# Kernel tuning notes

Hardware: AMD Instinct MI355X
Metric: run time of the kernel (lower is better)

Reference implementation:

```python
import jax, jax.numpy as jnp
import numpy as np

N = 50          # n_nodes
TAU = 1.0       # sinkhorn_tau
ITERS = 5       # sinkhorn_iters
ALPHA = 1.0


def _psi_fn(x, W1, b1, W2, b2):
    # x: [B, N, F]
    h = jax.nn.leaky_relu(x @ W1 + b1)          # [B, N, H], slope 0.01 matches torch default
    M = jax.nn.leaky_relu(h @ W2 + b2)          # [B, N, N]
    P = jnp.exp(M / TAU)
    for _ in range(ITERS):                      # alternating row/col normalization
        P = P / jnp.sum(P, axis=2, keepdims=True)
        P = P / jnp.sum(P, axis=1, keepdims=True)
    return P


def _hungarian(cost):
    """O(n^3) Hungarian (shortest augmenting path, like scipy.linear_sum_assignment).
    cost: [n, n] numpy. Returns col index assigned to each row (minimizes cost)."""
    n = cost.shape[0]
    INF = 1e18
    u = np.zeros(n + 1)
    v = np.zeros(n + 1)
    p = np.zeros(n + 1, dtype=np.int64)   # p[j] = row matched to column j (1-based)
    for i in range(1, n + 1):
        p[0] = i
        j0 = 0
        minv = np.full(n + 1, INF)
        way = np.zeros(n + 1, dtype=np.int64)
        used = np.zeros(n + 1, dtype=bool)
        while True:
            used[j0] = True
            i0 = p[j0]
            cur = cost[i0 - 1, :] - u[i0] - v[1:]
            free = ~used[1:]
            better = free & (cur < minv[1:])
            mv = minv[1:]
            mv[better] = cur[better]
            way[1:][better] = j0
            cand = np.where(free, mv, INF)
            j1 = int(np.argmin(cand)) + 1
            delta = cand[j1 - 1]
            u[p[used]] += delta
            v[used] -= delta
            mv[free] -= delta
            j0 = j1
            if p[j0] == 0:
                break
        while j0 != 0:
            j1 = way[j0]
            p[j0] = p[j1]
            j0 = j1
    row_to_col = np.zeros(n, dtype=np.int64)
    for j in range(1, n + 1):
        if p[j] > 0:
            row_to_col[p[j] - 1] = j - 1
    return row_to_col


def setup_inputs() -> dict:
    key = jax.random.key(0)
    k1, k2, k3, k4, k5 = jax.random.split(key, 5)
    B, F, H = 128, 1024, 4096
    s1 = 1.0 / np.sqrt(F)
    s2 = 1.0 / np.sqrt(H)
    x = jax.random.normal(k1, (B, N, F), dtype=jnp.float32)
    W1 = jax.random.uniform(k2, (F, H), minval=-s1, maxval=s1, dtype=jnp.float32)
    b1 = jax.random.uniform(k3, (H,), minval=-s1, maxval=s1, dtype=jnp.float32)
    W2 = jax.random.uniform(k4, (H, N), minval=-s2, maxval=s2, dtype=jnp.float32)
    b2 = jax.random.uniform(k5, (N,), minval=-s2, maxval=s2, dtype=jnp.float32)
    return {"x": x, "W1": W1, "b1": b1, "W2": W2, "b2": b2, "do_round": 1}


def reference(x, W1, b1, W2, b2, do_round):
    psi = _psi_fn(x, W1, b1, W2, b2)            # [B, N, N] doubly-stochastic (approx)
    if do_round:
        batch = np.asarray(psi)
        B = batch.shape[0]
        perms_np = np.zeros((B, N, N), dtype=np.float32)
        rows = np.arange(N)
        for i in range(B):
            cols = _hungarian(-batch[i])        # maximize psi == minimize -psi
            perms_np[i, rows, cols] = 1.0
        perms = jnp.asarray(perms_np)
        dist = jnp.sum(psi * perms, axis=(1, 2)) / N   # [B]
        X = (1.0 - ALPHA) * perms + ALPHA * psi
        return (psi, perms, X, dist)
    return (psi, None, None, None)
```

## Files before the change

### kernel.cpp

```cpp
#include <hip/hip_runtime.h>

#define NMAT 50
#define BATCH 128
#define FDIM 1024
#define HDIM 4096
#define ROWS 6400
#define PSIZE 320000
#define NPART 8
#define HINF 1e18

#define WS_M_OFF   0
#define WS_XH_OFF  20480000LL
#define WS_XL_OFF  33587200LL
#define WS_W1H_OFF 46694400LL
#define WS_W1L_OFF 55083008LL
#define WS_W2P_OFF 63471616LL
#define WS_H_OFF   64520192LL
#define WS_MIN     (WS_H_OFF + 128LL * HDIM * 4)

typedef __bf16 bf16x8 __attribute__((ext_vector_type(8)));
typedef float f32x4 __attribute__((ext_vector_type(4)));
typedef double f64x4 __attribute__((ext_vector_type(4)));
typedef unsigned short u16;

__device__ __forceinline__ float bf16_to_f32(unsigned short h) {
  return __uint_as_float(((unsigned int)h) << 16);
}
__device__ __forceinline__ unsigned short f32_to_bf16(float f) {
  unsigned int u = __float_as_uint(f);
  u += 0x7FFFu + ((u >> 16) & 1u);
  return (unsigned short)(u >> 16);
}

__device__ __forceinline__ void gload16(const u16* g, u16* l) {
  __builtin_amdgcn_global_load_lds(
      (const __attribute__((address_space(1))) unsigned int*)g,
      (__attribute__((address_space(3))) unsigned int*)l, 16, 0, 0);
}

__device__ __forceinline__ double wave_min_f64(double x) {
  union { double d; int i[2]; } u, t;
  u.d = x;
#define DPP_MIN_STEP(ctrl)                                                   \
  t.i[0] = __builtin_amdgcn_update_dpp(u.i[0], u.i[0], ctrl, 0xf, 0xf, false);\
  t.i[1] = __builtin_amdgcn_update_dpp(u.i[1], u.i[1], ctrl, 0xf, 0xf, false);\
  u.d = fmin(u.d, t.d);
  DPP_MIN_STEP(0x111)
  DPP_MIN_STEP(0x112)
  DPP_MIN_STEP(0x114)
  DPP_MIN_STEP(0x118)
  DPP_MIN_STEP(0x142)
  DPP_MIN_STEP(0x143)
#undef DPP_MIN_STEP
  union { double d; int i[2]; } r;
  r.i[0] = __builtin_amdgcn_readlane(u.i[0], 63);
  r.i[1] = __builtin_amdgcn_readlane(u.i[1], 63);
  return r.d;
}

__global__ __launch_bounds__(256) void convert_x(
    const float* __restrict__ X, u16* __restrict__ Xh, u16* __restrict__ Xl) {
  int t = threadIdx.x;
  int mt = blockIdx.x >> 5, k0b = blockIdx.x & 31;
  size_t outbase = (size_t)blockIdx.x * 4096;
#pragma unroll
  for (int it = 0; it < 2; ++it) {
    int idx = t + it * 256;
    int m = idx & 127, kg = idx >> 7;
    const float* src = X + (size_t)(mt * 128 + m) * FDIM + k0b * 32 + kg * 8;
    float4 v0 = *(const float4*)src;
    float4 v1 = *(const float4*)(src + 4);
    float f[8] = {v0.x, v0.y, v0.z, v0.w, v1.x, v1.y, v1.z, v1.w};
    unsigned short h[8], l[8];
#pragma unroll
    for (int j = 0; j < 8; ++j) {
      h[j] = f32_to_bf16(f[j]);
      l[j] = f32_to_bf16(f[j] - bf16_to_f32(h[j]));
    }
    uint4 hv, lv;
    hv.x = h[0] | ((unsigned)h[1] << 16); hv.y = h[2] | ((unsigned)h[3] << 16);
    hv.z = h[4] | ((unsigned)h[5] << 16); hv.w = h[6] | ((unsigned)h[7] << 16);
    lv.x = l[0] | ((unsigned)l[1] << 16); lv.y = l[2] | ((unsigned)l[3] << 16);
    lv.z = l[4] | ((unsigned)l[5] << 16); lv.w = l[6] | ((unsigned)l[7] << 16);
    size_t off = outbase + (size_t)(kg * 128 + m) * 8;
    *(uint4*)&Xh[off] = hv;
    *(uint4*)&Xl[off] = lv;
  }
}

__global__ __launch_bounds__(256) void convert_w1(
    const float* __restrict__ W1, u16* __restrict__ Wh, u16* __restrict__ Wl) {
  int t = threadIdx.x;
  int nt = blockIdx.x >> 5, k0b = blockIdx.x & 31;
  size_t outbase = (size_t)blockIdx.x * 4096;
#pragma unroll
  for (int it = 0; it < 2; ++it) {
    int idx = t + it * 256;
    int n = idx & 127, kg = idx >> 7;
    float f[8];
#pragma unroll
    for (int j = 0; j < 8; ++j)
      f[j] = W1[(size_t)(k0b * 32 + kg * 8 + j) * HDIM + nt * 128 + n];
    unsigned short h[8], l[8];
#pragma unroll
    for (int j = 0; j < 8; ++j) {
      h[j] = f32_to_bf16(f[j]);
      l[j] = f32_to_bf16(f[j] - bf16_to_f32(h[j]));
    }
    uint4 hv, lv;
    hv.x = h[0] | ((unsigned)h[1] << 16); hv.y = h[2] | ((unsigned)h[3] << 16);
    hv.z = h[4] | ((unsigned)h[5] << 16); hv.w = h[6] | ((unsigned)h[7] << 16);
    lv.x = l[0] | ((unsigned)l[1] << 16); lv.y = l[2] | ((unsigned)l[3] << 16);
    lv.z = l[4] | ((unsigned)l[5] << 16); lv.w = l[6] | ((unsigned)l[7] << 16);
    size_t off = outbase + (size_t)(kg * 128 + n) * 8;
    *(uint4*)&Wh[off] = hv;
    *(uint4*)&Wl[off] = lv;
  }
}

__global__ __launch_bounds__(256) void convert_w2(
    const float* __restrict__ W2, float* __restrict__ W2p) {
  int idx = blockIdx.x * 256 + threadIdx.x;
  int k = idx >> 6, n = idx & 63;
  W2p[idx] = (n < NMAT) ? W2[(size_t)k * NMAT + n] : 0.0f;
}

__global__ __launch_bounds__(256) void gemm1_mfma(
    const u16* __restrict__ Ah_, const u16* __restrict__ Al_,
    const u16* __restrict__ Bh_, const u16* __restrict__ Bl_,
    const float* __restrict__ b1,
    float* __restrict__ HTout,
    int mt0, int stride) {
  __shared__ __align__(16) u16 Ah[4096];
  __shared__ __align__(16) u16 Al[4096];
  __shared__ __align__(16) u16 Bh[4096];
  __shared__ __align__(16) u16 Bl[4096];
  int t = threadIdx.x;
  int wave = t >> 6, lane = t & 63;
  int nt = blockIdx.x & 31;
  int mtl = blockIdx.x >> 5;
  int wm = wave >> 1, wn = wave & 1;
  int fr = lane & 15, fg = lane >> 4;

  f32x4 acc[4][4];
#pragma unroll
  for (int i = 0; i < 4; ++i)
#pragma unroll
    for (int j = 0; j < 4; ++j) acc[i][j] = (f32x4){0.f, 0.f, 0.f, 0.f};

  const u16* pAh = Ah_ + (size_t)(mt0 + mtl) * 32 * 4096;
  const u16* pAl = Al_ + (size_t)(mt0 + mtl) * 32 * 4096;
  const u16* pBh = Bh_ + (size_t)nt * 32 * 4096;
  const u16* pBl = Bl_ + (size_t)nt * 32 * 4096;
  int so = wave * 1024 + lane * 8;
  int ld = wave * 1024;

  for (int k0b = 0; k0b < 32; ++k0b) {
    __syncthreads();
    size_t sb = (size_t)k0b * 4096;
    gload16(pAh + sb + so,       &Ah[ld]);
    gload16(pAh + sb + so + 512, &Ah[ld + 512]);
    gload16(pAl + sb + so,       &Al[ld]);
    gload16(pAl + sb + so + 512, &Al[ld + 512]);
    gload16(pBh + sb + so,       &Bh[ld]);
    gload16(pBh + sb + so + 512, &Bh[ld + 512]);
    gload16(pBl + sb + so,       &Bl[ld]);
    gload16(pBl + sb + so + 512, &Bl[ld + 512]);
    __syncthreads();
    bf16x8 ah[4], al[4], bh[4], bl[4];
#pragma unroll
    for (int i = 0; i < 4; ++i) {
      int arow = (fg * 128 + wm * 64 + i * 16 + fr) * 8;
      ah[i] = *(const bf16x8*)&Ah[arow];
      al[i] = *(const bf16x8*)&Al[arow];
      int brow = (fg * 128 + wn * 64 + i * 16 + fr) * 8;
      bh[i] = *(const bf16x8*)&Bh[brow];
      bl[i] = *(const bf16x8*)&Bl[brow];
    }
#pragma unroll
    for (int i = 0; i < 4; ++i)
#pragma unroll
      for (int j = 0; j < 4; ++j)
        acc[i][j] = __builtin_amdgcn_mfma_f32_16x16x32_bf16(ah[i], bh[j], acc[i][j], 0, 0, 0);
#pragma unroll
    for (int i = 0; i < 4; ++i)
#pragma unroll
      for (int j = 0; j < 4; ++j)
        acc[i][j] = __builtin_amdgcn_mfma_f32_16x16x32_bf16(ah[i], bl[j], acc[i][j], 0, 0, 0);
#pragma unroll
    for (int i = 0; i < 4; ++i)
#pragma unroll
      for (int j = 0; j < 4; ++j)
        acc[i][j] = __builtin_amdgcn_mfma_f32_16x16x32_bf16(al[i], bh[j], acc[i][j], 0, 0, 0);
  }

  int colb = nt * 128 + wn * 64 + fr;
  int rowb = mtl * 128 + wm * 64 + fg * 4;
#pragma unroll
  for (int j = 0; j < 4; ++j) {
    float bias = b1[colb + j * 16];
#pragma unroll
    for (int i = 0; i < 4; ++i) {
      float4 v4;
      float* vp = &v4.x;
#pragma unroll
      for (int r = 0; r < 4; ++r) {
        float v = acc[i][j][r] + bias;
        vp[r] = v >= 0.0f ? v : 0.01f * v;
      }
      *(float4*)&HTout[(size_t)(colb + j * 16) * stride + rowb + i * 16] = v4;
    }
  }
}

__global__ __launch_bounds__(64) void gemm2_mfma(
    const float* __restrict__ hT,
    const float* __restrict__ W2p,
    double* __restrict__ Mpart,
    int row0, int stride) {
  int lane = threadIdx.x;
  int kz = blockIdx.y;
  int fr = lane & 15, fk = lane >> 4;

  f64x4 z4 = (f64x4){0.0, 0.0, 0.0, 0.0};
  f64x4 pA = __builtin_amdgcn_mfma_f64_16x16x4f64((double)lane, 1.0, z4, 0, 0, 0);
  f64x4 pB = __builtin_amdgcn_mfma_f64_16x16x4f64(1.0, (double)lane, z4, 0, 0, 0);
  int aAlt = ((int)pA[0]) & 3;
  int bAlt = ((int)pB[0]) & 3;
  int ai = aAlt ? (lane >> 2) : fr;
  int ak = aAlt ? (lane & 3) : fk;
  int bj = bAlt ? (lane >> 2) : fr;
  int bk = bAlt ? (lane & 3) : fk;
  f64x4 p1 = __builtin_amdgcn_mfma_f64_16x16x4f64((double)ai, 1.0, z4, 0, 0, 0);
  f64x4 p2 = __builtin_amdgcn_mfma_f64_16x16x4f64(1.0, (double)bj, z4, 0, 0, 0);
  int di[4], dj[4];
#pragma unroll
  for (int r = 0; r < 4; ++r) {
    di[r] = (((int)p1[r]) >> 2) & 15;
    dj[r] = (((int)p2[r]) >> 2) & 15;
  }

  f64x4 acc[4];
#pragma unroll
  for (int nt = 0; nt < 4; ++nt) acc[nt] = z4;

  const float* hA = hT + blockIdx.x * 16 + ai;
  const int kend = kz * (FDIM * 4 / NPART) + (FDIM * 4 / NPART);
#pragma unroll 4
  for (int k = kz * (FDIM * 4 / NPART); k < kend; k += 4) {
    double av = (double)hA[(size_t)(k + ak) * stride];
#pragma unroll
    for (int nt = 0; nt < 4; ++nt) {
      double bv = (double)W2p[(k + bk) * 64 + nt * 16 + bj];
      acc[nt] = __builtin_amdgcn_mfma_f64_16x16x4f64(av, bv, acc[nt], 0, 0, 0);
    }
  }

  double* Mout = Mpart + (size_t)kz * PSIZE;
  int rowbase = row0 + blockIdx.x * 16;
#pragma unroll
  for (int nt = 0; nt < 4; ++nt)
#pragma unroll
    for (int r = 0; r < 4; ++r) {
      int col = nt * 16 + dj[r];
      if (col < NMAT)
        Mout[(size_t)(rowbase + di[r]) * NMAT + col] = acc[nt][r];
    }
}

__global__ __launch_bounds__(64) void sinkhorn_hungarian(
    const double* __restrict__ Mpart, const float* __restrict__ b2,
    float* __restrict__ out_psi, float* __restrict__ out_X,
    float* __restrict__ out_perms, float* __restrict__ out_dist) {
  int b = blockIdx.x, lane = threadIdx.x;
  __shared__ double P[2500];
  __shared__ double cost[2500];
  __shared__ double rs[50];
  __shared__ double u[51];
  __shared__ int p[51];
  __shared__ int wayl[51];
  const size_t base = (size_t)b * 2500;

  for (int e = lane; e < 2500; e += 64) {
    double m = 0.0;
#pragma unroll
    for (int pz = 0; pz < NPART; ++pz)
      m += Mpart[(size_t)pz * PSIZE + base + e];
    m += (double)b2[e % 50];
    m = m >= 0.0 ? m : 0.01 * m;
    P[e] = exp(m);
  }
  __syncthreads();
  for (int it = 0; it < 5; ++it) {
    if (lane < 50) { double s = 0; for (int j = 0; j < 50; ++j) s += P[lane * 50 + j]; rs[lane] = s; }
    __syncthreads();
    for (int e = lane; e < 2500; e += 64) P[e] /= rs[e / 50];
    __syncthreads();
    if (lane < 50) { double s = 0; for (int r = 0; r < 50; ++r) s += P[r * 50 + lane]; rs[lane] = s; }
    __syncthreads();
    for (int e = lane; e < 2500; e += 64) P[e] /= rs[e % 50];
    __syncthreads();
  }
  for (int e = lane; e < 2500; e += 64) {
    float f = (float)P[e];
    out_psi[base + e] = f;
    out_X[base + e] = f;
    cost[e] = -P[e];
  }
  if (lane < 51) { u[lane] = 0.0; p[lane] = 0; }
  __syncthreads();

  double v = 0.0;
  bool lactive = lane < NMAT;
  for (int i = 1; i <= NMAT; ++i) {
    bool used = false;
    int way = 0;
    int j0 = 0, j1 = 0;
    for (int guard = 0; guard < 64; ++guard) {
      if (lane == j0 - 1) used = true;
      int i0 = (j0 == 0) ? i : p[j0];
      double ui0 = u[i0];
      double cand = HINF;
      if (lactive && !used) {
        cand = cost[(i0 - 1) * NMAT + lane] - ui0 - v;
        way = j0;
      }
      double m = wave_min_f64(cand);
      unsigned long long bal = __ballot(cand == m);
      j1 = (int)__builtin_ctzll(bal) + 1;
      double delta = m;
      __syncthreads();
      if (used) { v -= delta; u[p[lane + 1]] += delta; }
      if (lane == 63) u[i] += delta;
      __syncthreads();
      j0 = j1;
      if (p[j0] == 0) break;
    }
    if (lactive) wayl[lane + 1] = way;
    __syncthreads();
    if (lane == 0) {
      int j = j1;
      for (int step = 0; step < 64 && j != 0; ++step) {
        int jw = wayl[j];
        p[j] = (jw == 0) ? i : p[jw];
        j = jw;
      }
    }
    __syncthreads();
  }

  size_t pbase = (size_t)b * 2500;
  for (int e = lane; e < 2500; e += 64) out_perms[pbase + e] = 0.0f;
  __syncthreads();
  double val = 0.0;
  if (lactive) {
    int row = p[lane + 1] - 1;
    if (row < 0) row = 0;
    if (row > 49) row = 49;
    out_perms[pbase + (size_t)row * NMAT + lane] = 1.0f;
    val = P[(size_t)row * NMAT + lane];
  }
#pragma unroll
  for (int s = 32; s > 0; s >>= 1) val += __shfl_xor(val, s, 64);
  if (lane == 0) out_dist[b] = (float)(val / (double)NMAT);
}

extern "C" void kernel_launch(void* const* d_in, const int* in_sizes, int n_in,
                              void* d_out, int out_size, void* d_ws, size_t ws_size,
                              hipStream_t stream) {
  const float* x  = (const float*)d_in[0];
  const float* W1 = (const float*)d_in[1];
  const float* b1 = (const float*)d_in[2];
  const float* W2 = (const float*)d_in[3];
  const float* b2 = (const float*)d_in[4];
  float* out = (float*)d_out;
  float* out_psi   = out;
  float* out_perms = out + PSIZE;
  float* out_X     = out + 2 * PSIZE;
  float* out_dist  = out + 3 * PSIZE;

  if (ws_size < (size_t)WS_MIN) return;

  char* ws = (char*)d_ws;
  double* Mpart = (double*)(ws + WS_M_OFF);
  u16* Xh  = (u16*)(ws + WS_XH_OFF);
  u16* Xl  = (u16*)(ws + WS_XL_OFF);
  u16* W1h = (u16*)(ws + WS_W1H_OFF);
  u16* W1l = (u16*)(ws + WS_W1L_OFF);
  float* W2p  = (float*)(ws + WS_W2P_OFF);
  float* hbuf = (float*)(ws + WS_H_OFF);
  long long avail = (long long)ws_size - WS_H_OFF;
  int max_rows = (int)(avail / (HDIM * 4));
  max_rows = (max_rows / 128) * 128;
  if (max_rows > ROWS) max_rows = ROWS;

  hipLaunchKernelGGL(convert_x, dim3(1600), dim3(256), 0, stream, x, Xh, Xl);
  hipLaunchKernelGGL(convert_w1, dim3(1024), dim3(256), 0, stream, W1, W1h, W1l);
  hipLaunchKernelGGL(convert_w2, dim3(1024), dim3(256), 0, stream, W2, W2p);

  for (int r0 = 0; r0 < ROWS; r0 += max_rows) {
    int rows = (ROWS - r0 < max_rows) ? (ROWS - r0) : max_rows;
    hipLaunchKernelGGL(gemm1_mfma, dim3((rows / 128) * 32), dim3(256), 0, stream,
                       Xh, Xl, W1h, W1l, b1, hbuf, r0 / 128, rows);
    hipLaunchKernelGGL(gemm2_mfma, dim3(rows / 16, NPART), dim3(64), 0, stream,
                       hbuf, W2p, Mpart, r0, rows);
  }
  hipLaunchKernelGGL(sinkhorn_hungarian, dim3(BATCH), dim3(64), 0, stream,
                     Mpart, b2, out_psi, out_X, out_perms, out_dist);
}
```

Before: 561.2 us.

## Replace FP64 second GEMM with split-bf16 MFMA and float partial sums

The second GEMM moves from f64 16x16x4 MFMA to a three-term split-bf16 scheme (hi*hi, hi*lo, lo*hi) on bf16 16x16x32 MFMA. The first GEMM's epilogue now packs each hidden activation as a hi/lo bf16 pair in one 32-bit word, and W2 is pre-split and transposed to a K-contiguous layout. Partial results are stored in float instead of double, and the K split drops from 8 to 4 parts, which shrinks workspace traffic. The cost is lower accuracy, since the lo*lo term is dropped and partials are float, and that could change Hungarian assignments on near-ties.

```diff
diff --git a/kernel.cpp b/kernel.cpp
--- a/kernel.cpp
+++ b/kernel.cpp
@@ -6,22 +6,24 @@
 #define HDIM 4096
 #define ROWS 6400
 #define PSIZE 320000
-#define NPART 8
+#define NPART 4
 #define HINF 1e18
 
 #define WS_M_OFF   0
-#define WS_XH_OFF  20480000LL
-#define WS_XL_OFF  33587200LL
-#define WS_W1H_OFF 46694400LL
-#define WS_W1L_OFF 55083008LL
-#define WS_W2P_OFF 63471616LL
-#define WS_H_OFF   64520192LL
+#define WS_XH_OFF  5120000LL
+#define WS_XL_OFF  18227200LL
+#define WS_W1H_OFF 31334400LL
+#define WS_W1L_OFF 39723008LL
+#define WS_W2H_OFF 48111616LL
+#define WS_W2L_OFF 48635904LL
+#define WS_H_OFF   49160192LL
 #define WS_MIN     (WS_H_OFF + 128LL * HDIM * 4)
 
 typedef __bf16 bf16x8 __attribute__((ext_vector_type(8)));
+typedef short short8 __attribute__((ext_vector_type(8)));
 typedef float f32x4 __attribute__((ext_vector_type(4)));
-typedef double f64x4 __attribute__((ext_vector_type(4)));
 typedef unsigned short u16;
+typedef unsigned int u32;
 
 __device__ __forceinline__ float bf16_to_f32(unsigned short h) {
   return __uint_as_float(((unsigned int)h) << 16);
@@ -119,17 +121,21 @@
 }
 
 __global__ __launch_bounds__(256) void convert_w2(
-    const float* __restrict__ W2, float* __restrict__ W2p) {
+    const float* __restrict__ W2, u16* __restrict__ W2h, u16* __restrict__ W2l) {
   int idx = blockIdx.x * 256 + threadIdx.x;
-  int k = idx >> 6, n = idx & 63;
-  W2p[idx] = (n < NMAT) ? W2[(size_t)k * NMAT + n] : 0.0f;
+  int n = idx >> 12, k = idx & 4095;
+  float f = (n < NMAT) ? W2[(size_t)k * NMAT + n] : 0.0f;
+  unsigned short hi = f32_to_bf16(f);
+  unsigned short lo = f32_to_bf16(f - bf16_to_f32(hi));
+  W2h[idx] = hi;
+  W2l[idx] = lo;
 }
 
 __global__ __launch_bounds__(256) void gemm1_mfma(
     const u16* __restrict__ Ah_, const u16* __restrict__ Al_,
     const u16* __restrict__ Bh_, const u16* __restrict__ Bl_,
     const float* __restrict__ b1,
-    float* __restrict__ HTout,
+    u32* __restrict__ HTout,
     int mt0, int stride) {
   __shared__ __align__(16) u16 Ah[4096];
   __shared__ __align__(16) u16 Al[4096];
@@ -201,75 +207,76 @@
     float bias = b1[colb + j * 16];
 #pragma unroll
     for (int i = 0; i < 4; ++i) {
-      float4 v4;
-      float* vp = &v4.x;
+      uint4 pk;
+      u32* pp = &pk.x;
 #pragma unroll
       for (int r = 0; r < 4; ++r) {
         float v = acc[i][j][r] + bias;
-        vp[r] = v >= 0.0f ? v : 0.01f * v;
+        v = v >= 0.0f ? v : 0.01f * v;
+        unsigned short hi = f32_to_bf16(v);
+        unsigned short lo = f32_to_bf16(v - bf16_to_f32(hi));
+        pp[r] = ((u32)hi << 16) | lo;
       }
-      *(float4*)&HTout[(size_t)(colb + j * 16) * stride + rowb + i * 16] = v4;
-    }
-  }
-}
-
-__global__ __launch_bounds__(64) void gemm2_mfma(
-    const float* __restrict__ hT,
-    const float* __restrict__ W2p,
-    double* __restrict__ Mpart,
+      *(uint4*)&HTout[(size_t)(colb + j * 16) * stride + rowb + i * 16] = pk;
+    }
+  }
+}
+
+__global__ __launch_bounds__(64) void gemm2_bf16(
+    const u32* __restrict__ hT,
+    const u16* __restrict__ W2h,
+    const u16* __restrict__ W2l,
+    float* __restrict__ Mpart,
     int row0, int stride) {
   int lane = threadIdx.x;
   int kz = blockIdx.y;
-  int fr = lane & 15, fk = lane >> 4;
-
-  f64x4 z4 = (f64x4){0.0, 0.0, 0.0, 0.0};
-  f64x4 pA = __builtin_amdgcn_mfma_f64_16x16x4f64((double)lane, 1.0, z4, 0, 0, 0);
-  f64x4 pB = __builtin_amdgcn_mfma_f64_16x16x4f64(1.0, (double)lane, z4, 0, 0, 0);
-  int aAlt = ((int)pA[0]) & 3;
-  int bAlt = ((int)pB[0]) & 3;
-  int ai = aAlt ? (lane >> 2) : fr;
-  int ak = aAlt ? (lane & 3) : fk;
-  int bj = bAlt ? (lane >> 2) : fr;
-  int bk = bAlt ? (lane & 3) : fk;
-  f64x4 p1 = __builtin_amdgcn_mfma_f64_16x16x4f64((double)ai, 1.0, z4, 0, 0, 0);
-  f64x4 p2 = __builtin_amdgcn_mfma_f64_16x16x4f64(1.0, (double)bj, z4, 0, 0, 0);
-  int di[4], dj[4];
-#pragma unroll
-  for (int r = 0; r < 4; ++r) {
-    di[r] = (((int)p1[r]) >> 2) & 15;
-    dj[r] = (((int)p2[r]) >> 2) & 15;
-  }
-
-  f64x4 acc[4];
-#pragma unroll
-  for (int nt = 0; nt < 4; ++nt) acc[nt] = z4;
-
-  const float* hA = hT + blockIdx.x * 16 + ai;
-  const int kend = kz * (FDIM * 4 / NPART) + (FDIM * 4 / NPART);
-#pragma unroll 4
-  for (int k = kz * (FDIM * 4 / NPART); k < kend; k += 4) {
-    double av = (double)hA[(size_t)(k + ak) * stride];
+  int fr = lane & 15, fg = lane >> 4;
+
+  f32x4 acc[4];
+#pragma unroll
+  for (int nt = 0; nt < 4; ++nt) acc[nt] = (f32x4){0.f, 0.f, 0.f, 0.f};
+
+  const u32* hA = hT + blockIdx.x * 16 + fr;
+  for (int ks = 0; ks < 32; ++ks) {
+    int k0 = kz * 1024 + ks * 32;
+    u32 hp[8];
+#pragma unroll
+    for (int kk = 0; kk < 8; ++kk)
+      hp[kk] = hA[(size_t)(k0 + fg * 8 + kk) * stride];
+    short8 hs, ls;
+#pragma unroll
+    for (int kk = 0; kk < 8; ++kk) {
+      hs[kk] = (short)(hp[kk] >> 16);
+      ls[kk] = (short)(hp[kk] & 0xffffu);
+    }
+    bf16x8 ah = *(bf16x8*)&hs;
+    bf16x8 al = *(bf16x8*)&ls;
 #pragma unroll
     for (int nt = 0; nt < 4; ++nt) {
-      double bv = (double)W2p[(k + bk) * 64 + nt * 16 + bj];
-      acc[nt] = __builtin_amdgcn_mfma_f64_16x16x4f64(av, bv, acc[nt], 0, 0, 0);
-    }
-  }
-
-  double* Mout = Mpart + (size_t)kz * PSIZE;
-  int rowbase = row0 + blockIdx.x * 16;
-#pragma unroll
-  for (int nt = 0; nt < 4; ++nt)
-#pragma unroll
-    for (int r = 0; r < 4; ++r) {
-      int col = nt * 16 + dj[r];
-      if (col < NMAT)
-        Mout[(size_t)(rowbase + di[r]) * NMAT + col] = acc[nt][r];
-    }
+      const size_t boff = (size_t)(nt * 16 + fr) * 4096 + k0 + fg * 8;
+      bf16x8 bh = *(const bf16x8*)&W2h[boff];
+      bf16x8 bl = *(const bf16x8*)&W2l[boff];
+      acc[nt] = __builtin_amdgcn_mfma_f32_16x16x32_bf16(ah, bh, acc[nt], 0, 0, 0);
+      acc[nt] = __builtin_amdgcn_mfma_f32_16x16x32_bf16(ah, bl, acc[nt], 0, 0, 0);
+      acc[nt] = __builtin_amdgcn_mfma_f32_16x16x32_bf16(al, bh, acc[nt], 0, 0, 0);
+    }
+  }
+
+  float* Mout = Mpart + (size_t)kz * PSIZE;
+  int rowbase = row0 + blockIdx.x * 16 + fg * 4;
+#pragma unroll
+  for (int nt = 0; nt < 4; ++nt) {
+    int col = nt * 16 + fr;
+    if (col < NMAT) {
+#pragma unroll
+      for (int r = 0; r < 4; ++r)
+        Mout[(size_t)(rowbase + r) * NMAT + col] = acc[nt][r];
+    }
+  }
 }
 
 __global__ __launch_bounds__(64) void sinkhorn_hungarian(
-    const double* __restrict__ Mpart, const float* __restrict__ b2,
+    const float* __restrict__ Mpart, const float* __restrict__ b2,
     float* __restrict__ out_psi, float* __restrict__ out_X,
     float* __restrict__ out_perms, float* __restrict__ out_dist) {
   int b = blockIdx.x, lane = threadIdx.x;
@@ -285,7 +292,7 @@
     double m = 0.0;
 #pragma unroll
     for (int pz = 0; pz < NPART; ++pz)
-      m += Mpart[(size_t)pz * PSIZE + base + e];
+      m += (double)Mpart[(size_t)pz * PSIZE + base + e];
     m += (double)b2[e % 50];
     m = m >= 0.0 ? m : 0.01 * m;
     P[e] = exp(m);
@@ -382,13 +389,14 @@
   if (ws_size < (size_t)WS_MIN) return;
 
   char* ws = (char*)d_ws;
-  double* Mpart = (double*)(ws + WS_M_OFF);
+  float* Mpart = (float*)(ws + WS_M_OFF);
   u16* Xh  = (u16*)(ws + WS_XH_OFF);
   u16* Xl  = (u16*)(ws + WS_XL_OFF);
   u16* W1h = (u16*)(ws + WS_W1H_OFF);
   u16* W1l = (u16*)(ws + WS_W1L_OFF);
-  float* W2p  = (float*)(ws + WS_W2P_OFF);
-  float* hbuf = (float*)(ws + WS_H_OFF);
+  u16* W2h = (u16*)(ws + WS_W2H_OFF);
+  u16* W2l = (u16*)(ws + WS_W2L_OFF);
+  u32* hbuf = (u32*)(ws + WS_H_OFF);
   long long avail = (long long)ws_size - WS_H_OFF;
   int max_rows = (int)(avail / (HDIM * 4));
   max_rows = (max_rows / 128) * 128;
@@ -396,14 +404,14 @@
 
   hipLaunchKernelGGL(convert_x, dim3(1600), dim3(256), 0, stream, x, Xh, Xl);
   hipLaunchKernelGGL(convert_w1, dim3(1024), dim3(256), 0, stream, W1, W1h, W1l);
-  hipLaunchKernelGGL(convert_w2, dim3(1024), dim3(256), 0, stream, W2, W2p);
+  hipLaunchKernelGGL(convert_w2, dim3(1024), dim3(256), 0, stream, W2, W2h, W2l);
 
   for (int r0 = 0; r0 < ROWS; r0 += max_rows) {
     int rows = (ROWS - r0 < max_rows) ? (ROWS - r0) : max_rows;
     hipLaunchKernelGGL(gemm1_mfma, dim3((rows / 128) * 32), dim3(256), 0, stream,
                        Xh, Xl, W1h, W1l, b1, hbuf, r0 / 128, rows);
-    hipLaunchKernelGGL(gemm2_mfma, dim3(rows / 16, NPART), dim3(64), 0, stream,
-                       hbuf, W2p, Mpart, r0, rows);
+    hipLaunchKernelGGL(gemm2_bf16, dim3(rows / 16, NPART), dim3(64), 0, stream,
+                       hbuf, W2h, W2l, Mpart, r0, rows);
   }
   hipLaunchKernelGGL(sinkhorn_hungarian, dim3(BATCH), dim3(64), 0, stream,
                      Mpart, b2, out_psi, out_X, out_perms, out_dist);
```

New measurement: 492.2 us. 12.3% less time.
